# Kernel tuning notes

Hardware: AMD Instinct MI355X
Metric: run time of the kernel (lower is better)

## Reference

```python
import jax, jax.numpy as jnp
import numpy as np

QMAX = 127.0

def _quantize_int8(x, axis):
    """Symmetric dynamic int8 quantization along `axis`. Returns (int8 values, fp32 scale)."""
    amax = jnp.max(jnp.abs(x), axis=axis, keepdims=True)
    scale = jnp.maximum(amax, 1e-8) / QMAX
    q = jnp.clip(jnp.round(x / scale), -QMAX, QMAX).astype(jnp.int8)
    return q, scale


def setup_inputs() -> dict:
    key = jax.random.key(0)
    kx, kw, kb = jax.random.split(key, 3)
    tokens, d_in, d_out = 4096, 4096, 16384
    x = jax.random.normal(kx, (tokens, d_in), dtype=jnp.float32)
    weight = jax.random.normal(kw, (d_out, d_in), dtype=jnp.float32) * (1.0 / np.sqrt(d_in))
    bias = jax.random.normal(kb, (d_out,), dtype=jnp.float32)
    return {"x": x, "weight": weight, "bias": bias}


def reference(x, weight, bias):
    # Quantize activations per-row (over in_features), weights per-output-column.
    xq, sx = _quantize_int8(x, axis=-1)            # [T, in] int8, [T, 1] scale
    wq, sw = _quantize_int8(weight.T, axis=0)      # [in, out] int8, [1, out] scale
    acc = jnp.matmul(xq, wq, preferred_element_type=jnp.int32)  # [T, out] int32
    out = acc.astype(jnp.float32) * sx * sw + bias
    return out
```

## Files before the change

### kernel.cpp

```cpp
#include <hip/hip_runtime.h>
#include <stdint.h>

typedef int   i32x4 __attribute__((ext_vector_type(4)));
typedef float f32x4 __attribute__((ext_vector_type(4)));

#define AS1 __attribute__((address_space(1)))
#define AS3 __attribute__((address_space(3)))
#define G2L16(gp, lp) __builtin_amdgcn_global_load_lds((const AS1 void*)(gp), (AS3 void*)(lp), 16, 0, 0)

template<int COLS>
__global__ __launch_bounds__(256)
void quant_rows_k(const float* __restrict__ src, int8_t* __restrict__ q,
                  float* __restrict__ scale)
{
    constexpr int PER = COLS / 256;
    static_assert(PER == 16, "pack assumes 16 elems/thread");
    const int row = blockIdx.x;
    const int t   = threadIdx.x;
    const float* s = src + (size_t)row * COLS + (size_t)t * PER;

    float v[PER];
    #pragma unroll
    for (int i = 0; i < PER; i += 4) {
        f32x4 x4 = *reinterpret_cast<const f32x4*>(s + i);
        v[i+0] = x4[0]; v[i+1] = x4[1]; v[i+2] = x4[2]; v[i+3] = x4[3];
    }
    float amax = 0.0f;
    #pragma unroll
    for (int i = 0; i < PER; ++i) amax = fmaxf(amax, fabsf(v[i]));

    #pragma unroll
    for (int off = 32; off > 0; off >>= 1)
        amax = fmaxf(amax, __shfl_xor(amax, off, 64));

    __shared__ float red[4];
    if ((t & 63) == 0) red[t >> 6] = amax;
    __syncthreads();
    amax = fmaxf(fmaxf(red[0], red[1]), fmaxf(red[2], red[3]));

    const float sc = fmaxf(amax, 1e-8f) / 127.0f;
    if (t == 0) scale[row] = sc;

    union { i32x4 v4; int8_t b[16]; } pk;
    #pragma unroll
    for (int i = 0; i < PER; ++i) {
        float r = rintf(v[i] / sc);
        r = fminf(127.0f, fmaxf(-127.0f, r));
        pk.b[i] = (int8_t)r;
    }
    *reinterpret_cast<i32x4*>(q + (size_t)row * COLS + (size_t)t * PER) = pk.v4;
}

#define BM 256
#define BN 256
#define BKB 128

__device__ __forceinline__ i32x4 mfma_i8(i32x4 a, i32x4 b, i32x4 c) {
    return __builtin_amdgcn_mfma_i32_16x16x64_i8(a, b, c, 0, 0, 0);
}
__device__ __forceinline__ i32x4 ldsld(const int8_t* p) {
    return *reinterpret_cast<const i32x4*>(p);
}
#define FENCE asm volatile("" ::: "memory")
#define BAR   do { FENCE; __builtin_amdgcn_s_barrier(); FENCE; } while (0)

template<bool ST>
__device__ __forceinline__ void tile_fn(
    const int8_t* __restrict__ aB, const int8_t* __restrict__ bB,
    int kc0, int kc1, i32x4 (&acc)[8][4],
    const int8_t* __restrict__ gA, const int8_t* __restrict__ gB,
    int8_t* lAn, int8_t* lBn,
    size_t r64, size_t r128, int t16)
{
    i32x4 A00 = ldsld(aB + 0*2048 + kc0);
    i32x4 A01 = ldsld(aB + 1*2048 + kc0);
    i32x4 A02 = ldsld(aB + 2*2048 + kc0);
    i32x4 A03 = ldsld(aB + 3*2048 + kc0);
    i32x4 B00 = ldsld(bB + 0*2048 + kc0);
    i32x4 B01 = ldsld(bB + 1*2048 + kc0);
    i32x4 B02 = ldsld(bB + 2*2048 + kc0);
    i32x4 B03 = ldsld(bB + 3*2048 + kc0);
    if (ST) {
        G2L16(gB,       lBn + t16);
        G2L16(gB + r64, lBn + 8192 + t16);
    }
    __builtin_amdgcn_s_setprio(1);
    acc[0][0] = mfma_i8(A00, B00, acc[0][0]);
    acc[1][0] = mfma_i8(A01, B00, acc[1][0]);
    acc[2][0] = mfma_i8(A02, B00, acc[2][0]);
    acc[3][0] = mfma_i8(A03, B00, acc[3][0]);
    acc[0][1] = mfma_i8(A00, B01, acc[0][1]);
    acc[1][1] = mfma_i8(A01, B01, acc[1][1]);
    acc[2][1] = mfma_i8(A02, B01, acc[2][1]);
    acc[3][1] = mfma_i8(A03, B01, acc[3][1]);
    acc[0][2] = mfma_i8(A00, B02, acc[0][2]);
    acc[1][2] = mfma_i8(A01, B02, acc[1][2]);
    acc[2][2] = mfma_i8(A02, B02, acc[2][2]);
    acc[3][2] = mfma_i8(A03, B02, acc[3][2]);
    acc[0][3] = mfma_i8(A00, B03, acc[0][3]);
    acc[1][3] = mfma_i8(A01, B03, acc[1][3]);
    acc[2][3] = mfma_i8(A02, B03, acc[2][3]);
    acc[3][3] = mfma_i8(A03, B03, acc[3][3]);
    __builtin_amdgcn_s_setprio(0);
    if (ST) asm volatile("s_waitcnt vmcnt(2)" ::: "memory");
    else    asm volatile("s_waitcnt vmcnt(0)" ::: "memory");
    BAR;
    i32x4 A10 = ldsld(aB + 4*2048 + kc0);
    i32x4 A11 = ldsld(aB + 5*2048 + kc0);
    i32x4 A12 = ldsld(aB + 6*2048 + kc0);
    i32x4 A13 = ldsld(aB + 7*2048 + kc0);
    i32x4 A20 = ldsld(aB + 0*2048 + kc1);
    i32x4 A21 = ldsld(aB + 1*2048 + kc1);
    i32x4 A22 = ldsld(aB + 2*2048 + kc1);
    i32x4 A23 = ldsld(aB + 3*2048 + kc1);
    i32x4 B10 = ldsld(bB + 0*2048 + kc1);
    i32x4 B11 = ldsld(bB + 1*2048 + kc1);
    i32x4 B12 = ldsld(bB + 2*2048 + kc1);
    i32x4 B13 = ldsld(bB + 3*2048 + kc1);
    if (ST) {
        G2L16(gB + 2*r64, lBn + 16384 + t16);
        G2L16(gB + 3*r64, lBn + 24576 + t16);
    }
    __builtin_amdgcn_s_setprio(1);
    acc[4][0] = mfma_i8(A10, B00, acc[4][0]);
    acc[5][0] = mfma_i8(A11, B00, acc[5][0]);
    acc[6][0] = mfma_i8(A12, B00, acc[6][0]);
    acc[7][0] = mfma_i8(A13, B00, acc[7][0]);
    acc[4][1] = mfma_i8(A10, B01, acc[4][1]);
    acc[5][1] = mfma_i8(A11, B01, acc[5][1]);
    acc[6][1] = mfma_i8(A12, B01, acc[6][1]);
    acc[7][1] = mfma_i8(A13, B01, acc[7][1]);
    acc[4][2] = mfma_i8(A10, B02, acc[4][2]);
    acc[5][2] = mfma_i8(A11, B02, acc[5][2]);
    acc[6][2] = mfma_i8(A12, B02, acc[6][2]);
    acc[7][2] = mfma_i8(A13, B02, acc[7][2]);
    acc[4][3] = mfma_i8(A10, B03, acc[4][3]);
    acc[5][3] = mfma_i8(A11, B03, acc[5][3]);
    acc[6][3] = mfma_i8(A12, B03, acc[6][3]);
    acc[7][3] = mfma_i8(A13, B03, acc[7][3]);
    __builtin_amdgcn_s_setprio(0);
    BAR;
    i32x4 A30 = ldsld(aB + 4*2048 + kc1);
    i32x4 A31 = ldsld(aB + 5*2048 + kc1);
    i32x4 A32 = ldsld(aB + 6*2048 + kc1);
    i32x4 A33 = ldsld(aB + 7*2048 + kc1);
    if (ST) {
        G2L16(gA,        lAn + t16);
        G2L16(gA + r128, lAn + 16384 + t16);
    }
    __builtin_amdgcn_s_setprio(1);
    acc[0][0] = mfma_i8(A20, B10, acc[0][0]);
    acc[1][0] = mfma_i8(A21, B10, acc[1][0]);
    acc[2][0] = mfma_i8(A22, B10, acc[2][0]);
    acc[3][0] = mfma_i8(A23, B10, acc[3][0]);
    acc[0][1] = mfma_i8(A20, B11, acc[0][1]);
    acc[1][1] = mfma_i8(A21, B11, acc[1][1]);
    acc[2][1] = mfma_i8(A22, B11, acc[2][1]);
    acc[3][1] = mfma_i8(A23, B11, acc[3][1]);
    acc[0][2] = mfma_i8(A20, B12, acc[0][2]);
    acc[1][2] = mfma_i8(A21, B12, acc[1][2]);
    acc[2][2] = mfma_i8(A22, B12, acc[2][2]);
    acc[3][2] = mfma_i8(A23, B12, acc[3][2]);
    acc[0][3] = mfma_i8(A20, B13, acc[0][3]);
    acc[1][3] = mfma_i8(A21, B13, acc[1][3]);
    acc[2][3] = mfma_i8(A22, B13, acc[2][3]);
    acc[3][3] = mfma_i8(A23, B13, acc[3][3]);
    __builtin_amdgcn_s_setprio(0);
    BAR;
    if (ST) {
        G2L16(gA + r64,        lAn + 8192 + t16);
        G2L16(gA + r128 + r64, lAn + 24576 + t16);
    }
    __builtin_amdgcn_s_setprio(1);
    acc[4][0] = mfma_i8(A30, B10, acc[4][0]);
    acc[5][0] = mfma_i8(A31, B10, acc[5][0]);
    acc[6][0] = mfma_i8(A32, B10, acc[6][0]);
    acc[7][0] = mfma_i8(A33, B10, acc[7][0]);
    acc[4][1] = mfma_i8(A30, B11, acc[4][1]);
    acc[5][1] = mfma_i8(A31, B11, acc[5][1]);
    acc[6][1] = mfma_i8(A32, B11, acc[6][1]);
    acc[7][1] = mfma_i8(A33, B11, acc[7][1]);
    acc[4][2] = mfma_i8(A30, B12, acc[4][2]);
    acc[5][2] = mfma_i8(A31, B12, acc[5][2]);
    acc[6][2] = mfma_i8(A32, B12, acc[6][2]);
    acc[7][2] = mfma_i8(A33, B12, acc[7][2]);
    acc[4][3] = mfma_i8(A30, B13, acc[4][3]);
    acc[5][3] = mfma_i8(A31, B13, acc[5][3]);
    acc[6][3] = mfma_i8(A32, B13, acc[6][3]);
    acc[7][3] = mfma_i8(A33, B13, acc[7][3]);
    __builtin_amdgcn_s_setprio(0);
    if (ST) asm volatile("s_waitcnt vmcnt(2)" ::: "memory");
    BAR;
}

__global__ __launch_bounds__(512, 2)
void gemm_i8_k(const int8_t* __restrict__ A,
               const int8_t* __restrict__ B,
               const float*  __restrict__ sx,
               const float*  __restrict__ sw,
               const float*  __restrict__ bias,
               float* __restrict__ C,
               int M, int N, int K)
{
    __shared__ int8_t lA[2][BM * BKB];
    __shared__ int8_t lB[2][BN * BKB];

    const int t    = threadIdx.x;
    const int lane = t & 63;
    const int wid  = t >> 6;
    const int wm   = wid >> 2;
    const int wn   = wid & 3;

    const int nwg = (int)gridDim.x;
    const int bid = (int)blockIdx.x;
    const int swz = ((nwg & 7) == 0) ? ((bid & 7) * (nwg >> 3) + (bid >> 3)) : bid;
    const int nbn = N / BN;
    const int bm  = swz / nbn;
    const int bn  = swz % nbn;

    const int fr  = lane & 15;
    const int c4  = lane >> 4;
    const int sw8 = fr & 7;
    const int kc0 = ((c4    ) ^ sw8) * 16;
    const int kc1 = ((c4 + 4) ^ sw8) * 16;
    const int8_t* aB0 = &lA[0][(wm * 128 + fr) * BKB];
    const int8_t* aB1 = &lA[1][(wm * 128 + fr) * BKB];
    const int8_t* bB0 = &lB[0][(wn * 64  + fr) * BKB];
    const int8_t* bB1 = &lB[1][(wn * 64  + fr) * BKB];

    const int srow = t >> 3;
    const int skc  = ((t & 7) ^ (srow & 7)) * 16;
    const int t16  = t * 16;
    const int8_t* pA = A + (size_t)(bm * BM + srow) * K + skc;
    const int8_t* pB = B + (size_t)(bn * BN + srow) * K + skc;
    const size_t r64  = (size_t)64  * K;
    const size_t r128 = (size_t)128 * K;

    G2L16(pB,              &lB[0][0]     + t16);
    G2L16(pB + r64,        &lB[0][8192]  + t16);
    G2L16(pB + 2*r64,      &lB[0][16384] + t16);
    G2L16(pB + 3*r64,      &lB[0][24576] + t16);
    G2L16(pA,              &lA[0][0]     + t16);
    G2L16(pA + r128,       &lA[0][16384] + t16);
    G2L16(pA + r64,        &lA[0][8192]  + t16);
    G2L16(pA + r128 + r64, &lA[0][24576] + t16);
    asm volatile("s_waitcnt vmcnt(2)" ::: "memory");
    BAR;

    i32x4 acc[8][4] = {};

    const int NT = K / BKB;
    for (int tt = 0; tt + 2 < NT; tt += 2) {
        const size_t ko1 = (size_t)(tt + 1) * BKB;
        tile_fn<true>(aB0, bB0, kc0, kc1, acc, pA + ko1, pB + ko1, &lA[1][0], &lB[1][0], r64, r128, t16);
        const size_t ko2 = (size_t)(tt + 2) * BKB;
        tile_fn<true>(aB1, bB1, kc0, kc1, acc, pA + ko2, pB + ko2, &lA[0][0], &lB[0][0], r64, r128, t16);
    }
    {
        const size_t ko1 = (size_t)(NT - 1) * BKB;
        tile_fn<true >(aB0, bB0, kc0, kc1, acc, pA + ko1, pB + ko1, &lA[1][0], &lB[1][0], r64, r128, t16);
        tile_fn<false>(aB1, bB1, kc0, kc1, acc, pA, pB, &lA[0][0], &lB[0][0], r64, r128, t16);
    }

    const int r0 = bm * BM + wm * 128 + (c4 << 2);
    const int c0 = bn * BN + wn * 64 + fr;
    #pragma unroll
    for (int ni = 0; ni < 4; ++ni) {
        const int c = c0 + ni * 16;
        const float swc = sw[c];
        const float bc  = bias[c];
        #pragma unroll
        for (int mi = 0; mi < 8; ++mi) {
            const int rb = r0 + mi * 16;
            #pragma unroll
            for (int j = 0; j < 4; ++j) {
                const int r = rb + j;
                C[(size_t)r * N + c] = (float)acc[mi][ni][j] * sx[r] * swc + bc;
            }
        }
    }
}

extern "C" void kernel_launch(void* const* d_in, const int* in_sizes, int n_in,
                              void* d_out, int out_size, void* d_ws, size_t ws_size,
                              hipStream_t stream) {
    const float* x    = (const float*)d_in[0];
    const float* w    = (const float*)d_in[1];
    const float* bias = (const float*)d_in[2];
    float* out = (float*)d_out;

    const int dout   = in_sizes[2];
    const int din    = in_sizes[1] / dout;
    const int tokens = in_sizes[0] / din;

    char* ws = (char*)d_ws;
    float*  sx = (float*)ws;
    float*  sw = (float*)(ws + 16384);
    int8_t* xq = (int8_t*)(ws + 16384 + 65536);
    int8_t* wq = xq + (size_t)tokens * din;

    quant_rows_k<4096><<<tokens, 256, 0, stream>>>(x, xq, sx);
    quant_rows_k<4096><<<dout,   256, 0, stream>>>(w, wq, sw);

    const int grid = (tokens / BM) * (dout / BN);
    gemm_i8_k<<<grid, 512, 0, stream>>>(xq, wq, sx, sw, bias, out, tokens, dout, din);
}
```

Before: 415.6 us.

## Merge int8 GEMM tile schedule from four barrier phases into two

```diff
diff --git a/kernel.cpp b/kernel.cpp
--- a/kernel.cpp
+++ b/kernel.cpp
@@ -55,7 +55,7 @@
 #define BN 256
 #define BKB 128
 
-__device__ __forceinline__ i32x4 mfma_i8(i32x4 a, i32x4 b, i32x4 c) {
+__device__ __forceinline__ i32x4 mfma16(i32x4 a, i32x4 b, i32x4 c) {
     return __builtin_amdgcn_mfma_i32_16x16x64_i8(a, b, c, 0, 0, 0);
 }
 __device__ __forceinline__ i32x4 ldsld(const int8_t* p) {
@@ -72,122 +72,112 @@
     int8_t* lAn, int8_t* lBn,
     size_t r64, size_t r128, int t16)
 {
+    if (ST) {
+        G2L16(gB,         lBn + t16);
+        G2L16(gB + r64,   lBn + 8192  + t16);
+        G2L16(gB + 2*r64, lBn + 16384 + t16);
+        G2L16(gB + 3*r64, lBn + 24576 + t16);
+    }
+    i32x4 B00 = ldsld(bB + 0*2048 + kc0);
+    i32x4 B01 = ldsld(bB + 1*2048 + kc0);
+    i32x4 B02 = ldsld(bB + 2*2048 + kc0);
+    i32x4 B03 = ldsld(bB + 3*2048 + kc0);
     i32x4 A00 = ldsld(aB + 0*2048 + kc0);
     i32x4 A01 = ldsld(aB + 1*2048 + kc0);
     i32x4 A02 = ldsld(aB + 2*2048 + kc0);
     i32x4 A03 = ldsld(aB + 3*2048 + kc0);
-    i32x4 B00 = ldsld(bB + 0*2048 + kc0);
-    i32x4 B01 = ldsld(bB + 1*2048 + kc0);
-    i32x4 B02 = ldsld(bB + 2*2048 + kc0);
-    i32x4 B03 = ldsld(bB + 3*2048 + kc0);
-    if (ST) {
-        G2L16(gB,       lBn + t16);
-        G2L16(gB + r64, lBn + 8192 + t16);
-    }
+    i32x4 B10 = ldsld(bB + 0*2048 + kc1);
+    i32x4 B11 = ldsld(bB + 1*2048 + kc1);
+    i32x4 B12 = ldsld(bB + 2*2048 + kc1);
+    i32x4 B13 = ldsld(bB + 3*2048 + kc1);
+    i32x4 A20 = ldsld(aB + 0*2048 + kc1);
+    i32x4 A21 = ldsld(aB + 1*2048 + kc1);
+    i32x4 A22 = ldsld(aB + 2*2048 + kc1);
+    i32x4 A23 = ldsld(aB + 3*2048 + kc1);
     __builtin_amdgcn_s_setprio(1);
-    acc[0][0] = mfma_i8(A00, B00, acc[0][0]);
-    acc[1][0] = mfma_i8(A01, B00, acc[1][0]);
-    acc[2][0] = mfma_i8(A02, B00, acc[2][0]);
-    acc[3][0] = mfma_i8(A03, B00, acc[3][0]);
-    acc[0][1] = mfma_i8(A00, B01, acc[0][1]);
-    acc[1][1] = mfma_i8(A01, B01, acc[1][1]);
-    acc[2][1] = mfma_i8(A02, B01, acc[2][1]);
-    acc[3][1] = mfma_i8(A03, B01, acc[3][1]);
-    acc[0][2] = mfma_i8(A00, B02, acc[0][2]);
-    acc[1][2] = mfma_i8(A01, B02, acc[1][2]);
-    acc[2][2] = mfma_i8(A02, B02, acc[2][2]);
-    acc[3][2] = mfma_i8(A03, B02, acc[3][2]);
-    acc[0][3] = mfma_i8(A00, B03, acc[0][3]);
-    acc[1][3] = mfma_i8(A01, B03, acc[1][3]);
-    acc[2][3] = mfma_i8(A02, B03, acc[2][3]);
-    acc[3][3] = mfma_i8(A03, B03, acc[3][3]);
+    acc[0][0] = mfma16(A00, B00, acc[0][0]);
+    acc[1][0] = mfma16(A01, B00, acc[1][0]);
+    acc[2][0] = mfma16(A02, B00, acc[2][0]);
+    acc[3][0] = mfma16(A03, B00, acc[3][0]);
+    acc[0][1] = mfma16(A00, B01, acc[0][1]);
+    acc[1][1] = mfma16(A01, B01, acc[1][1]);
+    acc[2][1] = mfma16(A02, B01, acc[2][1]);
+    acc[3][1] = mfma16(A03, B01, acc[3][1]);
+    acc[0][2] = mfma16(A00, B02, acc[0][2]);
+    acc[1][2] = mfma16(A01, B02, acc[1][2]);
+    acc[2][2] = mfma16(A02, B02, acc[2][2]);
+    acc[3][2] = mfma16(A03, B02, acc[3][2]);
+    acc[0][3] = mfma16(A00, B03, acc[0][3]);
+    acc[1][3] = mfma16(A01, B03, acc[1][3]);
+    acc[2][3] = mfma16(A02, B03, acc[2][3]);
+    acc[3][3] = mfma16(A03, B03, acc[3][3]);
+    acc[0][0] = mfma16(A20, B10, acc[0][0]);
+    acc[1][0] = mfma16(A21, B10, acc[1][0]);
+    acc[2][0] = mfma16(A22, B10, acc[2][0]);
+    acc[3][0] = mfma16(A23, B10, acc[3][0]);
+    acc[0][1] = mfma16(A20, B11, acc[0][1]);
+    acc[1][1] = mfma16(A21, B11, acc[1][1]);
+    acc[2][1] = mfma16(A22, B11, acc[2][1]);
+    acc[3][1] = mfma16(A23, B11, acc[3][1]);
+    acc[0][2] = mfma16(A20, B12, acc[0][2]);
+    acc[1][2] = mfma16(A21, B12, acc[1][2]);
+    acc[2][2] = mfma16(A22, B12, acc[2][2]);
+    acc[3][2] = mfma16(A23, B12, acc[3][2]);
+    acc[0][3] = mfma16(A20, B13, acc[0][3]);
+    acc[1][3] = mfma16(A21, B13, acc[1][3]);
+    acc[2][3] = mfma16(A22, B13, acc[2][3]);
+    acc[3][3] = mfma16(A23, B13, acc[3][3]);
     __builtin_amdgcn_s_setprio(0);
-    if (ST) asm volatile("s_waitcnt vmcnt(2)" ::: "memory");
+    if (ST) asm volatile("s_waitcnt vmcnt(4)" ::: "memory");
     else    asm volatile("s_waitcnt vmcnt(0)" ::: "memory");
     BAR;
+    if (ST) {
+        G2L16(gA,              lAn + t16);
+        G2L16(gA + r128,       lAn + 16384 + t16);
+        G2L16(gA + r64,        lAn + 8192  + t16);
+        G2L16(gA + r128 + r64, lAn + 24576 + t16);
+    }
     i32x4 A10 = ldsld(aB + 4*2048 + kc0);
     i32x4 A11 = ldsld(aB + 5*2048 + kc0);
     i32x4 A12 = ldsld(aB + 6*2048 + kc0);
     i32x4 A13 = ldsld(aB + 7*2048 + kc0);
-    i32x4 A20 = ldsld(aB + 0*2048 + kc1);
-    i32x4 A21 = ldsld(aB + 1*2048 + kc1);
-    i32x4 A22 = ldsld(aB + 2*2048 + kc1);
-    i32x4 A23 = ldsld(aB + 3*2048 + kc1);
-    i32x4 B10 = ldsld(bB + 0*2048 + kc1);
-    i32x4 B11 = ldsld(bB + 1*2048 + kc1);
-    i32x4 B12 = ldsld(bB + 2*2048 + kc1);
-    i32x4 B13 = ldsld(bB + 3*2048 + kc1);
-    if (ST) {
-        G2L16(gB + 2*r64, lBn + 16384 + t16);
-        G2L16(gB + 3*r64, lBn + 24576 + t16);
-    }
-    __builtin_amdgcn_s_setprio(1);
-    acc[4][0] = mfma_i8(A10, B00, acc[4][0]);
-    acc[5][0] = mfma_i8(A11, B00, acc[5][0]);
-    acc[6][0] = mfma_i8(A12, B00, acc[6][0]);
-    acc[7][0] = mfma_i8(A13, B00, acc[7][0]);
-    acc[4][1] = mfma_i8(A10, B01, acc[4][1]);
-    acc[5][1] = mfma_i8(A11, B01, acc[5][1]);
-    acc[6][1] = mfma_i8(A12, B01, acc[6][1]);
-    acc[7][1] = mfma_i8(A13, B01, acc[7][1]);
-    acc[4][2] = mfma_i8(A10, B02, acc[4][2]);
-    acc[5][2] = mfma_i8(A11, B02, acc[5][2]);
-    acc[6][2] = mfma_i8(A12, B02, acc[6][2]);
-    acc[7][2] = mfma_i8(A13, B02, acc[7][2]);
-    acc[4][3] = mfma_i8(A10, B03, acc[4][3]);
-    acc[5][3] = mfma_i8(A11, B03, acc[5][3]);
-    acc[6][3] = mfma_i8(A12, B03, acc[6][3]);
-    acc[7][3] = mfma_i8(A13, B03, acc[7][3]);
-    __builtin_amdgcn_s_setprio(0);
-    BAR;
     i32x4 A30 = ldsld(aB + 4*2048 + kc1);
     i32x4 A31 = ldsld(aB + 5*2048 + kc1);
     i32x4 A32 = ldsld(aB + 6*2048 + kc1);
     i32x4 A33 = ldsld(aB + 7*2048 + kc1);
-    if (ST) {
-        G2L16(gA,        lAn + t16);
-        G2L16(gA + r128, lAn + 16384 + t16);
-    }
     __builtin_amdgcn_s_setprio(1);
-    acc[0][0] = mfma_i8(A20, B10, acc[0][0]);
-    acc[1][0] = mfma_i8(A21, B10, acc[1][0]);
-    acc[2][0] = mfma_i8(A22, B10, acc[2][0]);
-    acc[3][0] = mfma_i8(A23, B10, acc[3][0]);
-    acc[0][1] = mfma_i8(A20, B11, acc[0][1]);
-    acc[1][1] = mfma_i8(A21, B11, acc[1][1]);
-    acc[2][1] = mfma_i8(A22, B11, acc[2][1]);
-    acc[3][1] = mfma_i8(A23, B11, acc[3][1]);
-    acc[0][2] = mfma_i8(A20, B12, acc[0][2]);
-    acc[1][2] = mfma_i8(A21, B12, acc[1][2]);
-    acc[2][2] = mfma_i8(A22, B12, acc[2][2]);
-    acc[3][2] = mfma_i8(A23, B12, acc[3][2]);
-    acc[0][3] = mfma_i8(A20, B13, acc[0][3]);
-    acc[1][3] = mfma_i8(A21, B13, acc[1][3]);
-    acc[2][3] = mfma_i8(A22, B13, acc[2][3]);
-    acc[3][3] = mfma_i8(A23, B13, acc[3][3]);
-    __builtin_amdgcn_s_setprio(0);
-    BAR;
-    if (ST) {
-        G2L16(gA + r64,        lAn + 8192 + t16);
-        G2L16(gA + r128 + r64, lAn + 24576 + t16);
-    }
-    __builtin_amdgcn_s_setprio(1);
-    acc[4][0] = mfma_i8(A30, B10, acc[4][0]);
-    acc[5][0] = mfma_i8(A31, B10, acc[5][0]);
-    acc[6][0] = mfma_i8(A32, B10, acc[6][0]);
-    acc[7][0] = mfma_i8(A33, B10, acc[7][0]);
-    acc[4][1] = mfma_i8(A30, B11, acc[4][1]);
-    acc[5][1] = mfma_i8(A31, B11, acc[5][1]);
-    acc[6][1] = mfma_i8(A32, B11, acc[6][1]);
-    acc[7][1] = mfma_i8(A33, B11, acc[7][1]);
-    acc[4][2] = mfma_i8(A30, B12, acc[4][2]);
-    acc[5][2] = mfma_i8(A31, B12, acc[5][2]);
-    acc[6][2] = mfma_i8(A32, B12, acc[6][2]);
-    acc[7][2] = mfma_i8(A33, B12, acc[7][2]);
-    acc[4][3] = mfma_i8(A30, B13, acc[4][3]);
-    acc[5][3] = mfma_i8(A31, B13, acc[5][3]);
-    acc[6][3] = mfma_i8(A32, B13, acc[6][3]);
-    acc[7][3] = mfma_i8(A33, B13, acc[7][3]);
+    acc[4][0] = mfma16(A10, B00, acc[4][0]);
+    acc[5][0] = mfma16(A11, B00, acc[5][0]);
+    acc[6][0] = mfma16(A12, B00, acc[6][0]);
+    acc[7][0] = mfma16(A13, B00, acc[7][0]);
+    acc[4][1] = mfma16(A10, B01, acc[4][1]);
+    acc[5][1] = mfma16(A11, B01, acc[5][1]);
+    acc[6][1] = mfma16(A12, B01, acc[6][1]);
+    acc[7][1] = mfma16(A13, B01, acc[7][1]);
+    acc[4][2] = mfma16(A10, B02, acc[4][2]);
+    acc[5][2] = mfma16(A11, B02, acc[5][2]);
+    acc[6][2] = mfma16(A12, B02, acc[6][2]);
+    acc[7][2] = mfma16(A13, B02, acc[7][2]);
+    acc[4][3] = mfma16(A10, B03, acc[4][3]);
+    acc[5][3] = mfma16(A11, B03, acc[5][3]);
+    acc[6][3] = mfma16(A12, B03, acc[6][3]);
+    acc[7][3] = mfma16(A13, B03, acc[7][3]);
+    acc[4][0] = mfma16(A30, B10, acc[4][0]);
+    acc[5][0] = mfma16(A31, B10, acc[5][0]);
+    acc[6][0] = mfma16(A32, B10, acc[6][0]);
+    acc[7][0] = mfma16(A33, B10, acc[7][0]);
+    acc[4][1] = mfma16(A30, B11, acc[4][1]);
+    acc[5][1] = mfma16(A31, B11, acc[5][1]);
+    acc[6][1] = mfma16(A32, B11, acc[6][1]);
+    acc[7][1] = mfma16(A33, B11, acc[7][1]);
+    acc[4][2] = mfma16(A30, B12, acc[4][2]);
+    acc[5][2] = mfma16(A31, B12, acc[5][2]);
+    acc[6][2] = mfma16(A32, B12, acc[6][2]);
+    acc[7][2] = mfma16(A33, B12, acc[7][2]);
+    acc[4][3] = mfma16(A30, B13, acc[4][3]);
+    acc[5][3] = mfma16(A31, B13, acc[5][3]);
+    acc[6][3] = mfma16(A32, B13, acc[6][3]);
+    acc[7][3] = mfma16(A33, B13, acc[7][3]);
     __builtin_amdgcn_s_setprio(0);
     if (ST) asm volatile("s_waitcnt vmcnt(2)" ::: "memory");
     BAR;
```

Result: slower. 445.6 us (+7.2%).
